# Kernel optimization log

Hardware: AMD Instinct MI355X
Metric: run time of the kernel (lower is better)

Reference implementation:

```python
import jax, jax.numpy as jnp
import numpy as np
import math

N, IFZ, NVZ, AHZ, QPZ, KZ, PEZ = 1024, 256, 64, 8, 4, 20, 20
NUM_FREQ = PEZ // 2
FREQ_INV = 50.0

def layer_norm(x, g, b, eps=1e-5):
    mu = x.mean(-1, keepdims=True)
    var = ((x - mu) ** 2).mean(-1, keepdims=True)
    return (x - mu) / jnp.sqrt(var + eps) * g + b

def setup_inputs() -> dict:
    key = jax.random.key(0)
    ks = jax.random.split(key, 8)
    x = jax.random.normal(ks[0], (N, IFZ), jnp.float32)
    affines = jax.random.normal(ks[1], (N, 3, 4), jnp.float32)
    prot_mask = jnp.ones((N,), dtype=bool)
    edge_index = jax.random.randint(ks[2], (N, KZ), 0, N, dtype=jnp.int32)
    s = 0.02
    w_nde = jax.random.normal(ks[3], (KZ * 3 * PEZ, NVZ), jnp.float32) * s
    b_nde = jnp.zeros((NVZ,), jnp.float32)
    w_q = jax.random.normal(ks[4], (IFZ + NVZ, AHZ * QPZ * 3), jnp.float32) * s
    w_v = jax.random.normal(ks[5], (IFZ + NVZ, AHZ * QPZ * IFZ), jnp.float32) * s
    ln_ag_g = jnp.ones((AHZ * QPZ * IFZ,), jnp.float32)
    ln_ag_b = jnp.zeros((AHZ * QPZ * IFZ,), jnp.float32)
    w_ag = jax.random.normal(ks[6], (AHZ * QPZ * IFZ, IFZ), jnp.float32) * s
    ln_en_g = jnp.ones((IFZ,), jnp.float32)
    ln_en_b = jnp.zeros((IFZ,), jnp.float32)
    return dict(x=x, affines=affines, prot_mask=prot_mask, edge_index=edge_index,
                w_nde=w_nde, b_nde=b_nde, w_q=w_q, w_v=w_v,
                ln_ag_g=ln_ag_g, ln_ag_b=ln_ag_b, w_ag=w_ag,
                ln_en_g=ln_en_g, ln_en_b=ln_en_b)

def reference(x, affines, prot_mask, edge_index, w_nde, b_nde, w_q, w_v,
              ln_ag_g, ln_ag_b, w_ag, ln_en_g, ln_en_b):
    dtype = x.dtype
    R = affines[:, :, :3]                                   # (N,3,3) rotation
    t = affines[:, :, 3]                                    # (N,3) translation
    positions = t
    # --- BackboneDistanceEmbedding (reconstructed): local neighbour vectors ---
    rel = positions[edge_index] - t[:, None, :]             # (N,K,3)
    local = jnp.einsum('nji,nkj->nki', R, rel)              # inverse-affine (R^T) (N,K,3)
    freqs = jnp.arange(1, NUM_FREQ + 1, dtype=dtype) / FREQ_INV
    ang = local[..., None] * freqs                          # (N,K,3,F)
    pe = jnp.concatenate([jnp.sin(ang), jnp.cos(ang)], -1)  # (N,K,3,PEZ)
    nv = jax.nn.relu(pe.reshape(x.shape[0], -1) @ w_nde + b_nde)  # (N,NVZ)
    nv = nv * prot_mask[:, None].astype(dtype)
    x_ne = jnp.concatenate([x, nv], axis=-1)                # (N,IFZ+NVZ)
    # --- query points in global frame ---
    q = (x_ne @ w_q).reshape(-1, 1, AHZ, QPZ, 3)
    q = jnp.einsum('nij,nkaqj->nkaqi', R, q) + t[:, None, None, None, :]
    gnp = positions[edge_index][:, :, None, None, :]        # (N,K,1,1,3)
    # --- L2-distance attention over neighbourhood ---
    scores = -jnp.linalg.norm(q - gnp, axis=-1).sum(-1)     # (N,K,AHZ)
    attn = jax.nn.softmax(scores, axis=1).astype(dtype)
    # --- value gather + weighted aggregation ---
    v = (x_ne @ w_v).reshape(-1, AHZ, QPZ, IFZ)
    v_ne = v[edge_index]                                    # (N,K,AHZ,QPZ,IFZ) -- big gather
    new = jnp.einsum('nkaqi,nka->naqi', v_ne, attn).reshape(x.shape[0], -1)
    new = layer_norm(new, ln_ag_g, ln_ag_b) @ w_ag          # dropout: eval mode => identity
    out = layer_norm(x + new / math.sqrt(2.0), ln_en_g, ln_en_b).astype(dtype)
    return out, edge_index
```

## Files before the change

### kernel.cpp

```cpp
#include <hip/hip_runtime.h>
#include <hip/hip_bf16.h>
#include <math.h>

#define NNODE 1024
#define IFZ   256
#define NVZ   64
#define AHZ   8
#define QPZ   4
#define KZ    20
#define NF    10
#define XNE   320
#define VROW  8192
#define PEK   1280
#define PTOT  2560

typedef unsigned short ushort;
typedef __attribute__((ext_vector_type(8))) short    short8v;
typedef __attribute__((ext_vector_type(8))) ushort   ushort8v;
typedef __attribute__((ext_vector_type(4))) float    float4v;

static __device__ __forceinline__ ushort f2bf(float f) {
    unsigned u = __float_as_uint(f);
    unsigned r = 0x7FFFu + ((u >> 16) & 1u);
    return (ushort)((u + r) >> 16);
}
static __device__ __forceinline__ float bf2f(unsigned h) {
    return __uint_as_float(h << 16);
}

struct Params {
    const float *w_ag, *ln_ag_g, *ln_ag_b, *w_nde, *b_nde, *w_q, *w_v, *x, *aff;
    const int   *edge;
    const float *ln_en_g, *ln_en_b;
    ushort *wagT, *wndeT, *wqT, *wv_bf, *pebf, *xne_bf, *agg, *WcT, *G;
    float  *rsum, *vpart, *vconst, *qbuf, *geom, *S, *s2part, *tmpk, *out;
};

static __device__ __forceinline__ void gemm_tile(
    const ushort* __restrict__ A, const ushort* __restrict__ BT,
    int aStride, int btStride, int kLen, int bm, int bn, int tid,
    float4v acc[2][2], ushort (&As)[64][40], ushort (&Bs)[64][40])
{
    const int w = tid >> 6, lane = tid & 63;
    const int wr = w >> 1, wc = w & 1;
    const int lane15 = lane & 15, quad = lane >> 4;
    const int sm = tid >> 2, sk = (tid & 3) * 8;
    for (int k0 = 0; k0 < kLen; k0 += 32) {
        *(ushort8v*)&As[sm][sk] = *(const ushort8v*)&A[(size_t)(bm + sm)*aStride + k0 + sk];
        *(ushort8v*)&Bs[sm][sk] = *(const ushort8v*)&BT[(size_t)(bn + sm)*btStride + k0 + sk];
        __syncthreads();
        short8v a0 = *(const short8v*)&As[wr*32      + lane15][quad*8];
        short8v a1 = *(const short8v*)&As[wr*32 + 16 + lane15][quad*8];
        short8v b0 = *(const short8v*)&Bs[wc*32      + lane15][quad*8];
        short8v b1 = *(const short8v*)&Bs[wc*32 + 16 + lane15][quad*8];
        acc[0][0] = __builtin_amdgcn_mfma_f32_16x16x32_bf16(a0, b0, acc[0][0], 0, 0, 0);
        acc[0][1] = __builtin_amdgcn_mfma_f32_16x16x32_bf16(a0, b1, acc[0][1], 0, 0, 0);
        acc[1][0] = __builtin_amdgcn_mfma_f32_16x16x32_bf16(a1, b0, acc[1][0], 0, 0, 0);
        acc[1][1] = __builtin_amdgcn_mfma_f32_16x16x32_bf16(a1, b1, acc[1][1], 0, 0, 0);
        __syncthreads();
    }
}

#define T1_END 2048
#define T2_END 2128
#define T3_END 2168
#define CV_END 2488
#define GV_END 2552
#define K0_END 2808

__global__ __launch_bounds__(256) void k_prep(Params P)
{
    const int u = blockIdx.x;
    const int tid = threadIdx.x;
    __shared__ float t[32][33];
    __shared__ float part[256];
    __shared__ float tn[4][KZ][3];
    __shared__ float r9[4][9], tt[4][3];

    if (u < T3_END) {
        const float* src; ushort* dst; const float* scl;
        int R, C, gx, Rdst, rel;
        if (u < T1_END)      { src=P.w_ag; dst=P.wagT; scl=P.ln_ag_g; R=VROW; C=IFZ; gx=8; Rdst=VROW; rel=u; }
        else if (u < T2_END) { src=P.w_nde;dst=P.wndeT;scl=nullptr;   R=1200; C=NVZ; gx=2; Rdst=PEK;  rel=u-T1_END; }
        else                 { src=P.w_q;  dst=P.wqT;  scl=nullptr;   R=XNE;  C=96;  gx=4; Rdst=XNE;  rel=u-T2_END; }
        const int bx = rel % gx, by = rel / gx;
        const int c0 = bx*32, r0 = by*32;
        const int tx = tid & 31, ty = tid >> 5;
        #pragma unroll
        for (int i = 0; i < 4; ++i) {
            int r = r0 + ty + 8*i, c = c0 + tx;
            float v = (r < R && c < C) ? src[(size_t)r * C + c] : 0.f;
            if (scl && r < R) v *= scl[r];
            t[ty + 8*i][tx] = v;
        }
        __syncthreads();
        #pragma unroll
        for (int i = 0; i < 4; ++i)
            dst[(size_t)(c0 + ty + 8*i) * Rdst + r0 + tx] = f2bf(t[tx][ty + 8*i]);
    } else if (u < CV_END) {
        const int j = u - T3_END;
        const float* src = P.w_v + (size_t)j*VROW + tid*32;
        ushort* dst = P.wv_bf + (size_t)j*VROW + tid*32;
        float psum = 0.f;
        #pragma unroll
        for (int q = 0; q < 4; ++q) {
            float4 v0 = ((const float4*)src)[q*2];
            float4 v1 = ((const float4*)src)[q*2+1];
            psum += v0.x+v0.y+v0.z+v0.w + v1.x+v1.y+v1.z+v1.w;
            ushort8v o;
            o[0]=f2bf(v0.x); o[1]=f2bf(v0.y); o[2]=f2bf(v0.z); o[3]=f2bf(v0.w);
            o[4]=f2bf(v1.x); o[5]=f2bf(v1.y); o[6]=f2bf(v1.z); o[7]=f2bf(v1.w);
            *(ushort8v*)(dst + q*8) = o;
        }
        part[tid] = psum;
        __syncthreads();
        if (tid < 8) {
            float s = 0.f;
            #pragma unroll
            for (int v = 0; v < 32; ++v) s += part[tid*32 + v];
            P.rsum[tid*320 + j] = s;
        }
    } else if (u < GV_END) {
        const int sp = u - CV_END, j = tid;
        const float* base = P.w_ag + (size_t)sp * 128 * IFZ;
        float vp = 0.f, bp = 0.f;
        for (int r = 0; r < 128; ++r) {
            float wv = base[(size_t)r * IFZ + j];
            vp += P.ln_ag_g[sp*128 + r] * wv;
            bp += P.ln_ag_b[sp*128 + r] * wv;
        }
        P.vpart[(size_t)(sp*2 + 0) * IFZ + j] = vp;
        P.vpart[(size_t)(sp*2 + 1) * IFZ + j] = bp;
    } else {
        const int rel = u - GV_END;
        const int wv = tid >> 6, lane = tid & 63;
        const int n = rel*4 + wv;
        if (lane < KZ) {
            int e = P.edge[n*KZ + lane];
            float a0 = P.aff[e*12 + 3], a1 = P.aff[e*12 + 7], a2 = P.aff[e*12 + 11];
            tn[wv][lane][0] = a0; tn[wv][lane][1] = a1; tn[wv][lane][2] = a2;
            P.geom[n*72 + 12 + lane*3 + 0] = a0;
            P.geom[n*72 + 12 + lane*3 + 1] = a1;
            P.geom[n*72 + 12 + lane*3 + 2] = a2;
        } else if (lane < 29) {
            int q = lane - 20;
            float v = P.aff[n*12 + (q/3)*4 + (q%3)];
            r9[wv][q] = v;
            P.geom[n*72 + q] = v;
        } else if (lane < 32) {
            float v = P.aff[n*12 + (lane-29)*4 + 3];
            tt[wv][lane-29] = v;
            P.geom[n*72 + 9 + (lane-29)] = v;
        }
        {
            float4 xv = ((const float4*)(P.x + (size_t)n*IFZ))[lane];
            unsigned lo = f2bf(xv.x) | ((unsigned)f2bf(xv.y) << 16);
            unsigned hi = f2bf(xv.z) | ((unsigned)f2bf(xv.w) << 16);
            unsigned* p = (unsigned*)(P.xne_bf + (size_t)n*XNE) + lane*2;
            p[0] = lo; p[1] = hi;
        }
        __syncthreads();
        if (lane < 60) {
            int k = lane / 3, i = lane % 3;
            float d0 = tn[wv][k][0]-tt[wv][0];
            float d1 = tn[wv][k][1]-tt[wv][1];
            float d2 = tn[wv][k][2]-tt[wv][2];
            float loc = r9[wv][0+i]*d0 + r9[wv][3+i]*d1 + r9[wv][6+i]*d2;
            size_t base = (size_t)n*PEK + k*60 + i*20;
            #pragma unroll
            for (int p = 0; p < NF; p += 2) {
                float a0 = loc * (float)(p+1) * (1.0f/50.0f);
                float a1 = loc * (float)(p+2) * (1.0f/50.0f);
                unsigned us = f2bf(__sinf(a0)) | ((unsigned)f2bf(__sinf(a1)) << 16);
                unsigned uc = f2bf(__cosf(a0)) | ((unsigned)f2bf(__cosf(a1)) << 16);
                *(unsigned*)&P.pebf[base + p]      = us;
                *(unsigned*)&P.pebf[base + 10 + p] = uc;
            }
        }
        if (lane < 40)
            *(unsigned*)&P.pebf[(size_t)n*PEK + 1200 + lane*2] = 0u;
    }
}

__global__ __launch_bounds__(256) void k_jobs(Params P)
{
    const int u = blockIdx.x;
    const int tid = threadIdx.x;
    __shared__ ushort As[64][40];
    __shared__ ushort Bs[64][40];

    if (u >= 408) {
        int vb = u - 408;
        float s = 0.f;
        #pragma unroll 8
        for (int sp = 0; sp < 64; ++sp)
            s += P.vpart[(size_t)(sp*2 + vb)*IFZ + tid];
        P.vconst[vb*IFZ + tid] = s;
        return;
    }
    const ushort *A, *BT;
    int aStr, btStr, kLen, bm, bn, mode, ldc;
    ushort* Cb = nullptr; float* Cf = nullptr; size_t cbase = 0;
    if (u < 160) {
        int bx=u%5, by=(u/5)%4, bz=u/20;
        A = P.wagT + bz*1024; BT = P.wv_bf + bz*1024;
        aStr=VROW; btStr=VROW; kLen=1024;
        bm=by*64; bn=bx*64; Cb=P.WcT; cbase=(size_t)bz*320; ldc=PTOT; mode=0;
    } else if (u < 360) {
        int rel=u-160; int bx=rel%5, by=(rel/5)%5, bz=rel/25;
        A = P.wv_bf + bz*1024; BT = P.wv_bf + bz*1024;
        aStr=VROW; btStr=VROW; kLen=1024;
        bm=by*64; bn=bx*64; Cb=P.G; cbase=(size_t)bz*102400; ldc=320; mode=0;
    } else if (u < 376) {
        int by=u-360;
        A = P.pebf; BT = P.wndeT; aStr=PEK; btStr=PEK; kLen=PEK;
        bm=by*64; bn=0; ldc=0; mode=2;
    } else {
        int rel=u-376; int bx=rel%2, by=rel/2;
        A = P.xne_bf; BT = P.wqT; aStr=XNE; btStr=XNE; kLen=256;
        bm=by*64; bn=bx*64; Cf=P.qbuf; cbase=0; ldc=128; mode=1;
    }
    float4v acc[2][2] = {};
    gemm_tile(A, BT, aStr, btStr, kLen, bm, bn, tid, acc, As, Bs);

    const int w = tid >> 6, lane = tid & 63;
    const int wr = w >> 1, wc = w & 1;
    const int lane15 = lane & 15, quad = lane >> 4;
    #pragma unroll
    for (int i = 0; i < 2; ++i) {
        #pragma unroll
        for (int j = 0; j < 2; ++j) {
            int col = bn + wc*32 + j*16 + lane15;
            #pragma unroll
            for (int r = 0; r < 4; ++r) {
                int row = bm + wr*32 + i*16 + quad*4 + r;
                float val = acc[i][j][r];
                if (mode == 2) {
                    val = fmaxf(val + P.b_nde[col], 0.f);
                    P.xne_bf[(size_t)row*XNE + IFZ + col] = f2bf(val);
                } else if (mode == 1) {
                    Cf[cbase + (size_t)row*ldc + col] = val;
                } else {
                    Cb[cbase + (size_t)row*ldc + col] = f2bf(val);
                }
            }
        }
    }
}

__global__ __launch_bounds__(256) void k_sc_agg(Params P)
{
    const int n = blockIdx.x;
    const int tid = threadIdx.x;
    __shared__ float geo[72], qf[96], qg[96], sc[160], at[160], nvr[64];
    __shared__ float rs[PTOT], red[256];
    __shared__ int es[KZ];
    __shared__ ushort xs[KZ][XNE];

    if (tid < 72) geo[tid] = P.geom[n*72 + tid];
    if (tid < KZ) es[tid] = P.edge[n*KZ + tid];
    if (tid < 64) nvr[tid] = bf2f(P.xne_bf[(size_t)n*XNE + IFZ + tid]);
    for (int p = tid; p < PTOT; p += 256) rs[p] = P.rsum[p];
    __syncthreads();

    for (int s = tid; s < KZ*40; s += 256) {
        int k = s / 40, ch = s % 40;
        *(ushort8v*)&xs[k][ch*8] =
            *(const ushort8v*)&P.xne_bf[(size_t)es[k]*XNE + ch*8];
    }
    if (tid < 96) {
        float qv = P.qbuf[n*128 + tid];
        #pragma unroll 16
        for (int r = 0; r < 64; ++r)
            qv += nvr[r] * P.w_q[(256 + r)*96 + tid];
        qf[tid] = qv;
    }
    __syncthreads();
    if (tid < 96) {
        int i = tid % 3, base = (tid/3)*3;
        qg[tid] = geo[i*3+0]*qf[base] + geo[i*3+1]*qf[base+1]
                + geo[i*3+2]*qf[base+2] + geo[9+i];
    }
    __syncthreads();
    if (tid < 160) {
        int k = tid / 8, a = tid % 8;
        float tx = geo[12+k*3+0], ty = geo[12+k*3+1], tz = geo[12+k*3+2];
        float acc = 0.f;
        #pragma unroll
        for (int qp = 0; qp < QPZ; ++qp) {
            int b = a*12 + qp*3;
            float dx = qg[b]   - tx;
            float dy = qg[b+1] - ty;
            float dz = qg[b+2] - tz;
            acc += sqrtf(dx*dx + dy*dy + dz*dz);
        }
        sc[a*20 + k] = -acc;
    }
    __syncthreads();
    if (tid < 8) {
        int a = tid;
        float m = -1e30f;
        #pragma unroll
        for (int k = 0; k < KZ; ++k) m = fmaxf(m, sc[a*20+k]);
        float e[KZ]; float sum = 0.f;
        #pragma unroll
        for (int k = 0; k < KZ; ++k) { e[k] = __expf(sc[a*20+k] - m); sum += e[k]; }
        float inv = 1.f / sum;
        #pragma unroll
        for (int k = 0; k < KZ; ++k) at[k*8 + a] = e[k]*inv;
    }
    __syncthreads();

    float sp = 0.f;
    for (int s = tid; s < AHZ*40; s += 256) {
        int a = s / 40, ch = s % 40;
        float acc[8] = {};
        #pragma unroll 4
        for (int k = 0; k < KZ; ++k) {
            ushort8v p = *(const ushort8v*)&xs[k][ch*8];
            float wgt = at[k*8 + a];
            #pragma unroll
            for (int j = 0; j < 8; ++j)
                acc[j] += wgt * bf2f((ushort)p[j]);
        }
        ushort8v o;
        #pragma unroll
        for (int j = 0; j < 8; ++j) {
            o[j] = (short)f2bf(acc[j]);
            sp += acc[j] * rs[a*320 + ch*8 + j];
        }
        *(ushort8v*)&P.agg[(size_t)n*PTOT + a*320 + ch*8] = o;
    }
    red[tid] = sp;
    __syncthreads();
    if (tid < 64) {
        float v = red[tid] + red[tid+64] + red[tid+128] + red[tid+192];
        #pragma unroll
        for (int off = 32; off > 0; off >>= 1) v += __shfl_down(v, off, 64);
        if (tid == 0) P.S[n] = v;
    }
}

__global__ __launch_bounds__(256) void k_gemm_b(Params P)
{
    const int u = blockIdx.x;
    const int tid = threadIdx.x;
    __shared__ ushort As[64][40];
    __shared__ ushort Bs[64][40];
    const int w = tid >> 6, lane = tid & 63;
    const int wr = w >> 1, wc = w & 1;
    const int lane15 = lane & 15, quad = lane >> 4;
    float4v acc[2][2] = {};

    if (u < 640) {
        const int bx = u % 5, by = (u/5) % 16, a = u/80;
        const int bm = by*64, bn = bx*64;
        gemm_tile(P.agg + a*320, P.G + (size_t)a*102400,
                  PTOT, 320, 320, bm, bn, tid, acc, As, Bs);
        #pragma unroll
        for (int i = 0; i < 2; ++i) {
            #pragma unroll
            for (int r = 0; r < 4; ++r) {
                int row = bm + wr*32 + i*16 + quad*4 + r;
                int c0  = bn + wc*32 + lane15;
                float av0 = bf2f(P.agg[(size_t)row*PTOT + a*320 + c0]);
                float av1 = bf2f(P.agg[(size_t)row*PTOT + a*320 + c0 + 16]);
                float v = acc[i][0][r]*av0 + acc[i][1][r]*av1;
                v += __shfl_xor(v, 1, 64);
                v += __shfl_xor(v, 2, 64);
                v += __shfl_xor(v, 4, 64);
                v += __shfl_xor(v, 8, 64);
                if (lane15 == 0)
                    P.s2part[(size_t)row*80 + a*10 + (bn>>5) + wc] = v;
            }
        }
    } else {
        const int rel = u - 640;
        const int bx = rel % 4, by = (rel/4) % 16, z = rel/64;
        const int bm = by*64, bn = bx*64;
        gemm_tile(P.agg + z*1280, P.WcT + z*1280,
                  PTOT, PTOT, 1280, bm, bn, tid, acc, As, Bs);
        float* Cf = P.tmpk + (size_t)z*NNODE*IFZ;
        #pragma unroll
        for (int i = 0; i < 2; ++i) {
            #pragma unroll
            for (int j = 0; j < 2; ++j) {
                int col = bn + wc*32 + j*16 + lane15;
                #pragma unroll
                for (int r = 0; r < 4; ++r) {
                    int row = bm + wr*32 + i*16 + quad*4 + r;
                    Cf[(size_t)row*IFZ + col] = acc[i][j][r];
                }
            }
        }
    }
}

__global__ __launch_bounds__(256) void k_final(Params P)
{
    const int n = blockIdx.x;
    const int tid = threadIdx.x;
    __shared__ float wsum[4], wsq[4];
    __shared__ float s_mu8, s_rstd8, s_mu, s_rstd;
    const int wid = tid >> 6, lane = tid & 63;

    float v = (tid < 80) ? P.s2part[(size_t)n*80 + tid] : 0.f;
    #pragma unroll
    for (int off = 32; off > 0; off >>= 1) v += __shfl_down(v, off, 64);
    if (lane == 0) wsum[wid] = v;
    __syncthreads();
    if (tid == 0) {
        float S2 = wsum[0]+wsum[1]+wsum[2]+wsum[3];
        float Sv = P.S[n];
        float mu = Sv * (1.f/(float)VROW);
        float var = S2 * (1.f/(float)VROW) - mu*mu;
        s_mu8 = mu; s_rstd8 = rsqrtf(var + 1e-5f);
    }
    __syncthreads();
    const float mu8 = s_mu8, rstd8 = s_rstd8;

    float s = P.tmpk[n*IFZ + tid] + P.tmpk[NNODE*IFZ + n*IFZ + tid];
    float vc = P.vconst[tid], bc = P.vconst[IFZ + tid];
    float pre = rstd8*s - rstd8*mu8*vc + bc;

    float val = P.x[n*IFZ + tid] + pre * 0.70710678118654752f;
    float lsum = val, lsq = val*val;
    #pragma unroll
    for (int off = 32; off > 0; off >>= 1) {
        lsum += __shfl_down(lsum, off, 64);
        lsq  += __shfl_down(lsq,  off, 64);
    }
    __syncthreads();
    if (lane == 0) { wsum[wid] = lsum; wsq[wid] = lsq; }
    __syncthreads();
    if (tid == 0) {
        float ts = wsum[0]+wsum[1]+wsum[2]+wsum[3];
        float tq = wsq[0]+wsq[1]+wsq[2]+wsq[3];
        float mu = ts / (float)IFZ;
        float var = tq / (float)IFZ - mu*mu;
        s_mu = mu; s_rstd = rsqrtf(var + 1e-5f);
    }
    __syncthreads();
    P.out[n*IFZ + tid] = (val - s_mu)*s_rstd*P.ln_en_g[tid] + P.ln_en_b[tid];
    if (tid < KZ)
        P.out[NNODE*IFZ + n*KZ + tid] = (float)P.edge[n*KZ + tid];
}

extern "C" void kernel_launch(void* const* d_in, const int* in_sizes, int n_in,
                              void* d_out, int out_size, void* d_ws, size_t ws_size,
                              hipStream_t stream)
{
    char* w = (char*)d_ws;
    Params P;
    P.x       = (const float*)d_in[0];
    P.aff     = (const float*)d_in[1];
    P.edge    = (const int*)d_in[3];
    P.w_nde   = (const float*)d_in[4];
    P.b_nde   = (const float*)d_in[5];
    P.w_q     = (const float*)d_in[6];
    P.w_v     = (const float*)d_in[7];
    P.ln_ag_g = (const float*)d_in[8];
    P.ln_ag_b = (const float*)d_in[9];
    P.w_ag    = (const float*)d_in[10];
    P.ln_en_g = (const float*)d_in[11];
    P.ln_en_b = (const float*)d_in[12];
    P.out     = (float*)d_out;

    P.xne_bf = (ushort*)(w + 0x0);
    P.qbuf   = (float*) (w + 0xA0000);
    P.vpart  = (float*) (w + 0x120000);
    P.vconst = (float*) (w + 0x140000);
    P.wagT   = (ushort*)(w + 0x250000);
    P.wv_bf  = (ushort*)(w + 0x650000);
    P.WcT    = (ushort*)(w + 0xB50000);
    P.G      = (ushort*)(w + 0xC90000);
    P.rsum   = (float*) (w + 0xE20000);
    P.S      = (float*) (w + 0xE23000);
    P.s2part = (float*) (w + 0xE24000);
    P.agg    = (ushort*)(w + 0xE80000);
    P.tmpk   = (float*) (w + 0x1380000);
    P.pebf   = (ushort*)(w + 0x1580000);
    P.wndeT  = (ushort*)(w + 0x1800000);
    P.wqT    = (ushort*)(w + 0x1828000);
    P.geom   = (float*) (w + 0x1840000);

    hipLaunchKernelGGL(k_prep,   dim3(K0_END), dim3(256), 0, stream, P);
    hipLaunchKernelGGL(k_jobs,   dim3(410),    dim3(256), 0, stream, P);
    hipLaunchKernelGGL(k_sc_agg, dim3(NNODE),  dim3(256), 0, stream, P);
    hipLaunchKernelGGL(k_gemm_b, dim3(768),    dim3(256), 0, stream, P);
    hipLaunchKernelGGL(k_final,  dim3(NNODE),  dim3(256), 0, stream, P);
}
```

Measured before the change: 161.3 us.

## Fuse node-embedding, query and attention softmax into prep kernel; merge launches

The positional-encoding MLP, query projection, global query transform, distance scores and softmax are now computed per group of four nodes inside k_prep with fp32 scalar loops, writing attention weights directly. This removes the bf16 PE buffer, the transposed w_nde/w_q copies, the qbuf/geom intermediates and their MFMA GEMM tiles. The aggregation work and the weight GEMMs are merged into a single k_mid launch, cutting one kernel launch and one global round trip. In exchange the PE and query matmuls run as scalar FMA loops over 256 blocks instead of tensor-core tiles, and each block reads the full w_nde and w_q.

```diff
diff --git a/kernel.cpp b/kernel.cpp
--- a/kernel.cpp
+++ b/kernel.cpp
@@ -11,7 +11,6 @@
 #define NF    10
 #define XNE   320
 #define VROW  8192
-#define PEK   1280
 #define PTOT  2560
 
 typedef unsigned short ushort;
@@ -32,8 +31,8 @@
     const float *w_ag, *ln_ag_g, *ln_ag_b, *w_nde, *b_nde, *w_q, *w_v, *x, *aff;
     const int   *edge;
     const float *ln_en_g, *ln_en_b;
-    ushort *wagT, *wndeT, *wqT, *wv_bf, *pebf, *xne_bf, *agg, *WcT, *G;
-    float  *rsum, *vpart, *vconst, *qbuf, *geom, *S, *s2part, *tmpk, *out;
+    ushort *xne_bf, *agg, *wagT, *wv_bf, *WcT, *G;
+    float  *rsum, *vpart, *vconst, *attn, *S, *s2part, *tmpk, *out;
 };
 
 static __device__ __forceinline__ void gemm_tile(
@@ -61,44 +60,166 @@
     }
 }
 
-#define T1_END 2048
-#define T2_END 2128
-#define T3_END 2168
-#define CV_END 2488
-#define GV_END 2552
-#define K0_END 2808
+#define K0P_END 256
+#define CV_END  576
+#define GV_END  640
+#define T1_END  2688
+
+union SharedP {
+    struct { float t[32][33]; } t1;
+    struct { float part[256]; } cv;
+    struct {
+        float tn[4][KZ][3], r9[4][9], tt[4][3];
+        float pe[4][1200];
+        float xr[4][IFZ];
+        float nv[4][NVZ];
+        float red[4][256];
+        float q[4][96];
+        float qred[2][384];
+        float qg[4][96];
+        float sc[4][160];
+    } k0;
+};
 
 __global__ __launch_bounds__(256) void k_prep(Params P)
 {
     const int u = blockIdx.x;
     const int tid = threadIdx.x;
-    __shared__ float t[32][33];
-    __shared__ float part[256];
-    __shared__ float tn[4][KZ][3];
-    __shared__ float r9[4][9], tt[4][3];
-
-    if (u < T3_END) {
-        const float* src; ushort* dst; const float* scl;
-        int R, C, gx, Rdst, rel;
-        if (u < T1_END)      { src=P.w_ag; dst=P.wagT; scl=P.ln_ag_g; R=VROW; C=IFZ; gx=8; Rdst=VROW; rel=u; }
-        else if (u < T2_END) { src=P.w_nde;dst=P.wndeT;scl=nullptr;   R=1200; C=NVZ; gx=2; Rdst=PEK;  rel=u-T1_END; }
-        else                 { src=P.w_q;  dst=P.wqT;  scl=nullptr;   R=XNE;  C=96;  gx=4; Rdst=XNE;  rel=u-T2_END; }
-        const int bx = rel % gx, by = rel / gx;
-        const int c0 = bx*32, r0 = by*32;
-        const int tx = tid & 31, ty = tid >> 5;
-        #pragma unroll
-        for (int i = 0; i < 4; ++i) {
-            int r = r0 + ty + 8*i, c = c0 + tx;
-            float v = (r < R && c < C) ? src[(size_t)r * C + c] : 0.f;
-            if (scl && r < R) v *= scl[r];
-            t[ty + 8*i][tx] = v;
-        }
-        __syncthreads();
-        #pragma unroll
-        for (int i = 0; i < 4; ++i)
-            dst[(size_t)(c0 + ty + 8*i) * Rdst + r0 + tx] = f2bf(t[tx][ty + 8*i]);
+    __shared__ SharedP sh;
+
+    if (u < K0P_END) {
+        const int n0 = u*4;
+        const int m = tid >> 6, lane = tid & 63;
+        const int n = n0 + m;
+
+        if (lane < KZ) {
+            int e = P.edge[n*KZ + lane];
+            sh.k0.tn[m][lane][0] = P.aff[e*12 + 3];
+            sh.k0.tn[m][lane][1] = P.aff[e*12 + 7];
+            sh.k0.tn[m][lane][2] = P.aff[e*12 + 11];
+        } else if (lane < 29) {
+            int q = lane - 20;
+            sh.k0.r9[m][q] = P.aff[n*12 + (q/3)*4 + (q%3)];
+        } else if (lane < 32) {
+            sh.k0.tt[m][lane-29] = P.aff[n*12 + (lane-29)*4 + 3];
+        }
+        {
+            float4 xv = ((const float4*)(P.x + (size_t)n*IFZ))[lane];
+            unsigned lo = f2bf(xv.x) | ((unsigned)f2bf(xv.y) << 16);
+            unsigned hi = f2bf(xv.z) | ((unsigned)f2bf(xv.w) << 16);
+            unsigned* p = (unsigned*)(P.xne_bf + (size_t)n*XNE) + lane*2;
+            p[0] = lo; p[1] = hi;
+            sh.k0.xr[m][lane*4+0] = xv.x; sh.k0.xr[m][lane*4+1] = xv.y;
+            sh.k0.xr[m][lane*4+2] = xv.z; sh.k0.xr[m][lane*4+3] = xv.w;
+        }
+        __syncthreads();
+
+        if (lane < 60) {
+            int k = lane / 3, i = lane % 3;
+            float d0 = sh.k0.tn[m][k][0]-sh.k0.tt[m][0];
+            float d1 = sh.k0.tn[m][k][1]-sh.k0.tt[m][1];
+            float d2 = sh.k0.tn[m][k][2]-sh.k0.tt[m][2];
+            float loc = sh.k0.r9[m][0+i]*d0 + sh.k0.r9[m][3+i]*d1 + sh.k0.r9[m][6+i]*d2;
+            int base = k*60 + i*20;
+            #pragma unroll
+            for (int p = 0; p < NF; ++p) {
+                float a = loc * (float)(p+1) * (1.0f/50.0f);
+                sh.k0.pe[m][base + p]      = __sinf(a);
+                sh.k0.pe[m][base + 10 + p] = __cosf(a);
+            }
+        }
+        __syncthreads();
+
+        {
+            const int c = tid & 63, chunk = tid >> 6;
+            const int r0 = chunk * 300;
+            float a0=0.f, a1=0.f, a2=0.f, a3=0.f;
+            for (int r = r0; r < r0 + 300; ++r) {
+                float wv = P.w_nde[r*NVZ + c];
+                a0 += sh.k0.pe[0][r]*wv;
+                a1 += sh.k0.pe[1][r]*wv;
+                a2 += sh.k0.pe[2][r]*wv;
+                a3 += sh.k0.pe[3][r]*wv;
+            }
+            sh.k0.red[chunk][0*64+c] = a0;
+            sh.k0.red[chunk][1*64+c] = a1;
+            sh.k0.red[chunk][2*64+c] = a2;
+            sh.k0.red[chunk][3*64+c] = a3;
+        }
+        __syncthreads();
+        {
+            const int mm = tid >> 6, c = tid & 63;
+            float nv = sh.k0.red[0][mm*64+c] + sh.k0.red[1][mm*64+c]
+                     + sh.k0.red[2][mm*64+c] + sh.k0.red[3][mm*64+c] + P.b_nde[c];
+            nv = fmaxf(nv, 0.f);
+            sh.k0.nv[mm][c] = nv;
+            P.xne_bf[(size_t)(n0+mm)*XNE + IFZ + c] = f2bf(nv);
+        }
+        __syncthreads();
+
+        if (tid < 192) {
+            const int chunk = tid / 96, j = tid - chunk*96;
+            const int rA = chunk*160, rB = rA + 160;
+            float q0=0.f, q1=0.f, q2=0.f, q3=0.f;
+            for (int r = rA; r < rB; ++r) {
+                float wq = P.w_q[r*96 + j];
+                float x0 = (r < IFZ) ? sh.k0.xr[0][r] : sh.k0.nv[0][r-IFZ];
+                float x1 = (r < IFZ) ? sh.k0.xr[1][r] : sh.k0.nv[1][r-IFZ];
+                float x2 = (r < IFZ) ? sh.k0.xr[2][r] : sh.k0.nv[2][r-IFZ];
+                float x3 = (r < IFZ) ? sh.k0.xr[3][r] : sh.k0.nv[3][r-IFZ];
+                q0 += x0*wq; q1 += x1*wq; q2 += x2*wq; q3 += x3*wq;
+            }
+            sh.k0.qred[chunk][0*96+j] = q0;
+            sh.k0.qred[chunk][1*96+j] = q1;
+            sh.k0.qred[chunk][2*96+j] = q2;
+            sh.k0.qred[chunk][3*96+j] = q3;
+        }
+        __syncthreads();
+        if (tid < 96) {
+            #pragma unroll
+            for (int mm = 0; mm < 4; ++mm)
+                sh.k0.q[mm][tid] = sh.k0.qred[0][mm*96+tid] + sh.k0.qred[1][mm*96+tid];
+        }
+        __syncthreads();
+
+        for (int c = lane; c < 96; c += 64) {
+            int i = c % 3, base = (c/3)*3;
+            sh.k0.qg[m][c] = sh.k0.r9[m][i*3+0]*sh.k0.q[m][base]
+                           + sh.k0.r9[m][i*3+1]*sh.k0.q[m][base+1]
+                           + sh.k0.r9[m][i*3+2]*sh.k0.q[m][base+2] + sh.k0.tt[m][i];
+        }
+        __syncthreads();
+
+        for (int s = lane; s < 160; s += 64) {
+            int k = s / 8, a = s % 8;
+            float tx = sh.k0.tn[m][k][0], ty = sh.k0.tn[m][k][1], tz = sh.k0.tn[m][k][2];
+            float acc = 0.f;
+            #pragma unroll
+            for (int qp = 0; qp < QPZ; ++qp) {
+                int b = a*12 + qp*3;
+                float dx = sh.k0.qg[m][b]   - tx;
+                float dy = sh.k0.qg[m][b+1] - ty;
+                float dz = sh.k0.qg[m][b+2] - tz;
+                acc += sqrtf(dx*dx + dy*dy + dz*dz);
+            }
+            sh.k0.sc[m][a*20 + k] = -acc;
+        }
+        __syncthreads();
+
+        if (lane < 8) {
+            int a = lane;
+            float mx = -1e30f;
+            #pragma unroll
+            for (int k = 0; k < KZ; ++k) mx = fmaxf(mx, sh.k0.sc[m][a*20+k]);
+            float e[KZ]; float sum = 0.f;
+            #pragma unroll
+            for (int k = 0; k < KZ; ++k) { e[k] = __expf(sh.k0.sc[m][a*20+k] - mx); sum += e[k]; }
+            float inv = 1.f / sum;
+            #pragma unroll
+            for (int k = 0; k < KZ; ++k) P.attn[n*160 + k*8 + a] = e[k]*inv;
+        }
     } else if (u < CV_END) {
-        const int j = u - T3_END;
+        const int j = u - K0P_END;
         const float* src = P.w_v + (size_t)j*VROW + tid*32;
         ushort* dst = P.wv_bf + (size_t)j*VROW + tid*32;
         float psum = 0.f;
@@ -112,12 +233,12 @@
             o[4]=f2bf(v1.x); o[5]=f2bf(v1.y); o[6]=f2bf(v1.z); o[7]=f2bf(v1.w);
             *(ushort8v*)(dst + q*8) = o;
         }
-        part[tid] = psum;
+        sh.cv.part[tid] = psum;
         __syncthreads();
         if (tid < 8) {
             float s = 0.f;
             #pragma unroll
-            for (int v = 0; v < 32; ++v) s += part[tid*32 + v];
+            for (int v = 0; v < 32; ++v) s += sh.cv.part[tid*32 + v];
             P.rsum[tid*320 + j] = s;
         }
     } else if (u < GV_END) {
@@ -133,64 +254,81 @@
         P.vpart[(size_t)(sp*2 + 1) * IFZ + j] = bp;
     } else {
         const int rel = u - GV_END;
-        const int wv = tid >> 6, lane = tid & 63;
-        const int n = rel*4 + wv;
-        if (lane < KZ) {
-            int e = P.edge[n*KZ + lane];
-            float a0 = P.aff[e*12 + 3], a1 = P.aff[e*12 + 7], a2 = P.aff[e*12 + 11];
-            tn[wv][lane][0] = a0; tn[wv][lane][1] = a1; tn[wv][lane][2] = a2;
-            P.geom[n*72 + 12 + lane*3 + 0] = a0;
-            P.geom[n*72 + 12 + lane*3 + 1] = a1;
-            P.geom[n*72 + 12 + lane*3 + 2] = a2;
-        } else if (lane < 29) {
-            int q = lane - 20;
-            float v = P.aff[n*12 + (q/3)*4 + (q%3)];
-            r9[wv][q] = v;
-            P.geom[n*72 + q] = v;
-        } else if (lane < 32) {
-            float v = P.aff[n*12 + (lane-29)*4 + 3];
-            tt[wv][lane-29] = v;
-            P.geom[n*72 + 9 + (lane-29)] = v;
-        }
-        {
-            float4 xv = ((const float4*)(P.x + (size_t)n*IFZ))[lane];
-            unsigned lo = f2bf(xv.x) | ((unsigned)f2bf(xv.y) << 16);
-            unsigned hi = f2bf(xv.z) | ((unsigned)f2bf(xv.w) << 16);
-            unsigned* p = (unsigned*)(P.xne_bf + (size_t)n*XNE) + lane*2;
-            p[0] = lo; p[1] = hi;
-        }
-        __syncthreads();
-        if (lane < 60) {
-            int k = lane / 3, i = lane % 3;
-            float d0 = tn[wv][k][0]-tt[wv][0];
-            float d1 = tn[wv][k][1]-tt[wv][1];
-            float d2 = tn[wv][k][2]-tt[wv][2];
-            float loc = r9[wv][0+i]*d0 + r9[wv][3+i]*d1 + r9[wv][6+i]*d2;
-            size_t base = (size_t)n*PEK + k*60 + i*20;
-            #pragma unroll
-            for (int p = 0; p < NF; p += 2) {
-                float a0 = loc * (float)(p+1) * (1.0f/50.0f);
-                float a1 = loc * (float)(p+2) * (1.0f/50.0f);
-                unsigned us = f2bf(__sinf(a0)) | ((unsigned)f2bf(__sinf(a1)) << 16);
-                unsigned uc = f2bf(__cosf(a0)) | ((unsigned)f2bf(__cosf(a1)) << 16);
-                *(unsigned*)&P.pebf[base + p]      = us;
-                *(unsigned*)&P.pebf[base + 10 + p] = uc;
-            }
-        }
-        if (lane < 40)
-            *(unsigned*)&P.pebf[(size_t)n*PEK + 1200 + lane*2] = 0u;
-    }
-}
-
-__global__ __launch_bounds__(256) void k_jobs(Params P)
+        const int bx = rel % 8, by = rel / 8;
+        const int c0 = bx*32, r0 = by*32;
+        const int tx = tid & 31, ty = tid >> 5;
+        #pragma unroll
+        for (int i = 0; i < 4; ++i) {
+            int r = r0 + ty + 8*i, c = c0 + tx;
+            sh.t1.t[ty + 8*i][tx] = P.w_ag[(size_t)r * IFZ + c] * P.ln_ag_g[r];
+        }
+        __syncthreads();
+        #pragma unroll
+        for (int i = 0; i < 4; ++i)
+            P.wagT[(size_t)(c0 + ty + 8*i) * VROW + r0 + tx] = f2bf(sh.t1.t[tx][ty + 8*i]);
+    }
+}
+
+union SharedM {
+    struct { ushort As[64][40]; ushort Bs[64][40]; } g;
+    struct { float at[160]; float rs[PTOT]; float red[256];
+             int es[KZ]; ushort xs[KZ][XNE]; } s;
+};
+
+__global__ __launch_bounds__(256) void k_mid(Params P)
 {
     const int u = blockIdx.x;
     const int tid = threadIdx.x;
-    __shared__ ushort As[64][40];
-    __shared__ ushort Bs[64][40];
-
-    if (u >= 408) {
-        int vb = u - 408;
+    __shared__ SharedM sh;
+
+    if (u < NNODE) {
+        const int n = u;
+        if (tid < 160) sh.s.at[tid] = P.attn[n*160 + tid];
+        if (tid < KZ) sh.s.es[tid] = P.edge[n*KZ + tid];
+        for (int p = tid; p < PTOT; p += 256) sh.s.rs[p] = P.rsum[p];
+        __syncthreads();
+
+        for (int s = tid; s < KZ*40; s += 256) {
+            int k = s / 40, ch = s % 40;
+            *(ushort8v*)&sh.s.xs[k][ch*8] =
+                *(const ushort8v*)&P.xne_bf[(size_t)sh.s.es[k]*XNE + ch*8];
+        }
+        __syncthreads();
+
+        float sp = 0.f;
+        for (int s = tid; s < AHZ*40; s += 256) {
+            int a = s / 40, ch = s % 40;
+            float acc[8] = {};
+            #pragma unroll 4
+            for (int k = 0; k < KZ; ++k) {
+                ushort8v p = *(const ushort8v*)&sh.s.xs[k][ch*8];
+                float wgt = sh.s.at[k*8 + a];
+                #pragma unroll
+                for (int j = 0; j < 8; ++j)
+                    acc[j] += wgt * bf2f((ushort)p[j]);
+            }
+            ushort8v o;
+            #pragma unroll
+            for (int j = 0; j < 8; ++j) {
+                o[j] = (short)f2bf(acc[j]);
+                sp += acc[j] * sh.s.rs[a*320 + ch*8 + j];
+            }
+            *(ushort8v*)&P.agg[(size_t)n*PTOT + a*320 + ch*8] = o;
+        }
+        sh.s.red[tid] = sp;
+        __syncthreads();
+        if (tid < 64) {
+            float v = sh.s.red[tid] + sh.s.red[tid+64] + sh.s.red[tid+128] + sh.s.red[tid+192];
+            #pragma unroll
+            for (int off = 32; off > 0; off >>= 1) v += __shfl_down(v, off, 64);
+            if (tid == 0) P.S[n] = v;
+        }
+        return;
+    }
+
+    const int u2 = u - NNODE;
+    if (u2 >= 360) {
+        int vb = u2 - 360;
         float s = 0.f;
         #pragma unroll 8
         for (int sp = 0; sp < 64; ++sp)
@@ -198,30 +336,18 @@
         P.vconst[vb*IFZ + tid] = s;
         return;
     }
-    const ushort *A, *BT;
-    int aStr, btStr, kLen, bm, bn, mode, ldc;
-    ushort* Cb = nullptr; float* Cf = nullptr; size_t cbase = 0;
-    if (u < 160) {
-        int bx=u%5, by=(u/5)%4, bz=u/20;
+    const ushort *A, *BT; ushort* Cb; size_t cbase; int bm, bn, ldc;
+    if (u2 < 160) {
+        int bx=u2%5, by=(u2/5)%4, bz=u2/20;
         A = P.wagT + bz*1024; BT = P.wv_bf + bz*1024;
-        aStr=VROW; btStr=VROW; kLen=1024;
-        bm=by*64; bn=bx*64; Cb=P.WcT; cbase=(size_t)bz*320; ldc=PTOT; mode=0;
-    } else if (u < 360) {
-        int rel=u-160; int bx=rel%5, by=(rel/5)%5, bz=rel/25;
+        bm=by*64; bn=bx*64; Cb=P.WcT; cbase=(size_t)bz*320; ldc=PTOT;
+    } else {
+        int rel=u2-160; int bx=rel%5, by=(rel/5)%5, bz=rel/25;
         A = P.wv_bf + bz*1024; BT = P.wv_bf + bz*1024;
-        aStr=VROW; btStr=VROW; kLen=1024;
-        bm=by*64; bn=bx*64; Cb=P.G; cbase=(size_t)bz*102400; ldc=320; mode=0;
-    } else if (u < 376) {
-        int by=u-360;
-        A = P.pebf; BT = P.wndeT; aStr=PEK; btStr=PEK; kLen=PEK;
-        bm=by*64; bn=0; ldc=0; mode=2;
-    } else {
-        int rel=u-376; int bx=rel%2, by=rel/2;
-        A = P.xne_bf; BT = P.wqT; aStr=XNE; btStr=XNE; kLen=256;
-        bm=by*64; bn=bx*64; Cf=P.qbuf; cbase=0; ldc=128; mode=1;
+        bm=by*64; bn=bx*64; Cb=P.G; cbase=(size_t)bz*102400; ldc=320;
     }
     float4v acc[2][2] = {};
-    gemm_tile(A, BT, aStr, btStr, kLen, bm, bn, tid, acc, As, Bs);
+    gemm_tile(A, BT, VROW, VROW, 1024, bm, bn, tid, acc, sh.g.As, sh.g.Bs);
 
     const int w = tid >> 6, lane = tid & 63;
     const int wr = w >> 1, wc = w & 1;
@@ -234,110 +360,9 @@
             #pragma unroll
             for (int r = 0; r < 4; ++r) {
                 int row = bm + wr*32 + i*16 + quad*4 + r;
-                float val = acc[i][j][r];
-                if (mode == 2) {
-                    val = fmaxf(val + P.b_nde[col], 0.f);
-                    P.xne_bf[(size_t)row*XNE + IFZ + col] = f2bf(val);
-                } else if (mode == 1) {
-                    Cf[cbase + (size_t)row*ldc + col] = val;
-                } else {
-                    Cb[cbase + (size_t)row*ldc + col] = f2bf(val);
-                }
-            }
-        }
-    }
-}
-
-__global__ __launch_bounds__(256) void k_sc_agg(Params P)
-{
-    const int n = blockIdx.x;
-    const int tid = threadIdx.x;
-    __shared__ float geo[72], qf[96], qg[96], sc[160], at[160], nvr[64];
-    __shared__ float rs[PTOT], red[256];
-    __shared__ int es[KZ];
-    __shared__ ushort xs[KZ][XNE];
-
-    if (tid < 72) geo[tid] = P.geom[n*72 + tid];
-    if (tid < KZ) es[tid] = P.edge[n*KZ + tid];
-    if (tid < 64) nvr[tid] = bf2f(P.xne_bf[(size_t)n*XNE + IFZ + tid]);
-    for (int p = tid; p < PTOT; p += 256) rs[p] = P.rsum[p];
-    __syncthreads();
-
-    for (int s = tid; s < KZ*40; s += 256) {
-        int k = s / 40, ch = s % 40;
-        *(ushort8v*)&xs[k][ch*8] =
-            *(const ushort8v*)&P.xne_bf[(size_t)es[k]*XNE + ch*8];
-    }
-    if (tid < 96) {
-        float qv = P.qbuf[n*128 + tid];
-        #pragma unroll 16
-        for (int r = 0; r < 64; ++r)
-            qv += nvr[r] * P.w_q[(256 + r)*96 + tid];
-        qf[tid] = qv;
-    }
-    __syncthreads();
-    if (tid < 96) {
-        int i = tid % 3, base = (tid/3)*3;
-        qg[tid] = geo[i*3+0]*qf[base] + geo[i*3+1]*qf[base+1]
-                + geo[i*3+2]*qf[base+2] + geo[9+i];
-    }
-    __syncthreads();
-    if (tid < 160) {
-        int k = tid / 8, a = tid % 8;
-        float tx = geo[12+k*3+0], ty = geo[12+k*3+1], tz = geo[12+k*3+2];
-        float acc = 0.f;
-        #pragma unroll
-        for (int qp = 0; qp < QPZ; ++qp) {
-            int b = a*12 + qp*3;
-            float dx = qg[b]   - tx;
-            float dy = qg[b+1] - ty;
-            float dz = qg[b+2] - tz;
-            acc += sqrtf(dx*dx + dy*dy + dz*dz);
-        }
-        sc[a*20 + k] = -acc;
-    }
-    __syncthreads();
-    if (tid < 8) {
-        int a = tid;
-        float m = -1e30f;
-        #pragma unroll
-        for (int k = 0; k < KZ; ++k) m = fmaxf(m, sc[a*20+k]);
-        float e[KZ]; float sum = 0.f;
-        #pragma unroll
-        for (int k = 0; k < KZ; ++k) { e[k] = __expf(sc[a*20+k] - m); sum += e[k]; }
-        float inv = 1.f / sum;
-        #pragma unroll
-        for (int k = 0; k < KZ; ++k) at[k*8 + a] = e[k]*inv;
-    }
-    __syncthreads();
-
-    float sp = 0.f;
-    for (int s = tid; s < AHZ*40; s += 256) {
-        int a = s / 40, ch = s % 40;
-        float acc[8] = {};
-        #pragma unroll 4
-        for (int k = 0; k < KZ; ++k) {
-            ushort8v p = *(const ushort8v*)&xs[k][ch*8];
-            float wgt = at[k*8 + a];
-            #pragma unroll
-            for (int j = 0; j < 8; ++j)
-                acc[j] += wgt * bf2f((ushort)p[j]);
-        }
-        ushort8v o;
-        #pragma unroll
-        for (int j = 0; j < 8; ++j) {
-            o[j] = (short)f2bf(acc[j]);
-            sp += acc[j] * rs[a*320 + ch*8 + j];
-        }
-        *(ushort8v*)&P.agg[(size_t)n*PTOT + a*320 + ch*8] = o;
-    }
-    red[tid] = sp;
-    __syncthreads();
-    if (tid < 64) {
-        float v = red[tid] + red[tid+64] + red[tid+128] + red[tid+192];
-        #pragma unroll
-        for (int off = 32; off > 0; off >>= 1) v += __shfl_down(v, off, 64);
-        if (tid == 0) P.S[n] = v;
+                Cb[cbase + (size_t)row*ldc + col] = f2bf(acc[i][j][r]);
+            }
+        }
     }
 }
 
@@ -467,26 +492,21 @@
     P.out     = (float*)d_out;
 
     P.xne_bf = (ushort*)(w + 0x0);
-    P.qbuf   = (float*) (w + 0xA0000);
-    P.vpart  = (float*) (w + 0x120000);
-    P.vconst = (float*) (w + 0x140000);
-    P.wagT   = (ushort*)(w + 0x250000);
-    P.wv_bf  = (ushort*)(w + 0x650000);
-    P.WcT    = (ushort*)(w + 0xB50000);
-    P.G      = (ushort*)(w + 0xC90000);
-    P.rsum   = (float*) (w + 0xE20000);
-    P.S      = (float*) (w + 0xE23000);
-    P.s2part = (float*) (w + 0xE24000);
-    P.agg    = (ushort*)(w + 0xE80000);
-    P.tmpk   = (float*) (w + 0x1380000);
-    P.pebf   = (ushort*)(w + 0x1580000);
-    P.wndeT  = (ushort*)(w + 0x1800000);
-    P.wqT    = (ushort*)(w + 0x1828000);
-    P.geom   = (float*) (w + 0x1840000);
-
-    hipLaunchKernelGGL(k_prep,   dim3(K0_END), dim3(256), 0, stream, P);
-    hipLaunchKernelGGL(k_jobs,   dim3(410),    dim3(256), 0, stream, P);
-    hipLaunchKernelGGL(k_sc_agg, dim3(NNODE),  dim3(256), 0, stream, P);
+    P.attn   = (float*) (w + 0xA0000);
+    P.vpart  = (float*) (w + 0x140000);
+    P.vconst = (float*) (w + 0x160000);
+    P.wagT   = (ushort*)(w + 0x170000);
+    P.wv_bf  = (ushort*)(w + 0x570000);
+    P.WcT    = (ushort*)(w + 0xA70000);
+    P.G      = (ushort*)(w + 0xBB0000);
+    P.rsum   = (float*) (w + 0xD40000);
+    P.S      = (float*) (w + 0xD43000);
+    P.s2part = (float*) (w + 0xD44000);
+    P.agg    = (ushort*)(w + 0xDA0000);
+    P.tmpk   = (float*) (w + 0x12A0000);
+
+    hipLaunchKernelGGL(k_prep,   dim3(T1_END), dim3(256), 0, stream, P);
+    hipLaunchKernelGGL(k_mid,    dim3(1386),   dim3(256), 0, stream, P);
     hipLaunchKernelGGL(k_gemm_b, dim3(768),    dim3(256), 0, stream, P);
     hipLaunchKernelGGL(k_final,  dim3(NNODE),  dim3(256), 0, stream, P);
 }
```

Result: slower. 171.0 us (+6.0%).

## Move weight-only GEMMs into the score/aggregation kernel to overlap work

Applied to the files above, without the earlier changes.

The weight-only GEMM tiles (WcT = w_ag^T·w_v and the Gram matrix G of w_v) no longer sit in the first jobs kernel. They now run as extra blocks of the per-node score/aggregation kernel, with shared memory overlaid through a union. The small jobs kernel keeps only the PE/NDE and query GEMMs plus the vconst reduction, so the critical path before aggregation gets shorter and the big GEMMs can run alongside the per-node blocks. The union shares the larger per-node shared-memory footprint with the GEMM blocks, which may limit occupancy. A small unroll pragma is also added to the vpart loop.

```diff
diff --git a/kernel.cpp b/kernel.cpp
--- a/kernel.cpp
+++ b/kernel.cpp
@@ -124,6 +124,7 @@
         const int sp = u - CV_END, j = tid;
         const float* base = P.w_ag + (size_t)sp * 128 * IFZ;
         float vp = 0.f, bp = 0.f;
+        #pragma unroll 4
         for (int r = 0; r < 128; ++r) {
             float wv = base[(size_t)r * IFZ + j];
             vp += P.ln_ag_g[sp*128 + r] * wv;
@@ -182,15 +183,15 @@
     }
 }
 
-__global__ __launch_bounds__(256) void k_jobs(Params P)
+__global__ __launch_bounds__(256) void k_sjobs(Params P)
 {
     const int u = blockIdx.x;
     const int tid = threadIdx.x;
     __shared__ ushort As[64][40];
     __shared__ ushort Bs[64][40];
 
-    if (u >= 408) {
-        int vb = u - 408;
+    if (u >= 48) {
+        int vb = u - 48;
         float s = 0.f;
         #pragma unroll 8
         for (int sp = 0; sp < 64; ++sp)
@@ -199,26 +200,14 @@
         return;
     }
     const ushort *A, *BT;
-    int aStr, btStr, kLen, bm, bn, mode, ldc;
-    ushort* Cb = nullptr; float* Cf = nullptr; size_t cbase = 0;
-    if (u < 160) {
-        int bx=u%5, by=(u/5)%4, bz=u/20;
-        A = P.wagT + bz*1024; BT = P.wv_bf + bz*1024;
-        aStr=VROW; btStr=VROW; kLen=1024;
-        bm=by*64; bn=bx*64; Cb=P.WcT; cbase=(size_t)bz*320; ldc=PTOT; mode=0;
-    } else if (u < 360) {
-        int rel=u-160; int bx=rel%5, by=(rel/5)%5, bz=rel/25;
-        A = P.wv_bf + bz*1024; BT = P.wv_bf + bz*1024;
-        aStr=VROW; btStr=VROW; kLen=1024;
-        bm=by*64; bn=bx*64; Cb=P.G; cbase=(size_t)bz*102400; ldc=320; mode=0;
-    } else if (u < 376) {
-        int by=u-360;
+    int kLen, bm, bn, mode, aStr, btStr;
+    if (u < 16) {
         A = P.pebf; BT = P.wndeT; aStr=PEK; btStr=PEK; kLen=PEK;
-        bm=by*64; bn=0; ldc=0; mode=2;
+        bm = u*64; bn = 0; mode = 2;
     } else {
-        int rel=u-376; int bx=rel%2, by=rel/2;
+        int rel = u - 16; int bx = rel % 2, by = rel / 2;
         A = P.xne_bf; BT = P.wqT; aStr=XNE; btStr=XNE; kLen=256;
-        bm=by*64; bn=bx*64; Cf=P.qbuf; cbase=0; ldc=128; mode=1;
+        bm = by*64; bn = bx*64; mode = 1;
     }
     float4v acc[2][2] = {};
     gemm_tile(A, BT, aStr, btStr, kLen, bm, bn, tid, acc, As, Bs);
@@ -238,76 +227,110 @@
                 if (mode == 2) {
                     val = fmaxf(val + P.b_nde[col], 0.f);
                     P.xne_bf[(size_t)row*XNE + IFZ + col] = f2bf(val);
-                } else if (mode == 1) {
-                    Cf[cbase + (size_t)row*ldc + col] = val;
                 } else {
-                    Cb[cbase + (size_t)row*ldc + col] = f2bf(val);
+                    P.qbuf[(size_t)row*128 + col] = val;
                 }
             }
         }
     }
 }
 
-__global__ __launch_bounds__(256) void k_sc_agg(Params P)
-{
-    const int n = blockIdx.x;
+union SharedM {
+    struct { ushort As[64][40]; ushort Bs[64][40]; } g;
+    struct { float geo[72], qf[96], qg[96], sc[160], at[160], nvr[64];
+             float rs[PTOT], red[256]; int es[KZ]; ushort xs[KZ][XNE]; } s;
+};
+
+__global__ __launch_bounds__(256) void k_mid(Params P)
+{
+    const int u = blockIdx.x;
     const int tid = threadIdx.x;
-    __shared__ float geo[72], qf[96], qg[96], sc[160], at[160], nvr[64];
-    __shared__ float rs[PTOT], red[256];
-    __shared__ int es[KZ];
-    __shared__ ushort xs[KZ][XNE];
-
-    if (tid < 72) geo[tid] = P.geom[n*72 + tid];
-    if (tid < KZ) es[tid] = P.edge[n*KZ + tid];
-    if (tid < 64) nvr[tid] = bf2f(P.xne_bf[(size_t)n*XNE + IFZ + tid]);
-    for (int p = tid; p < PTOT; p += 256) rs[p] = P.rsum[p];
+    __shared__ SharedM sh;
+
+    if (u < 360) {
+        const ushort *A, *BT; ushort* Cb; size_t cbase; int bm, bn, ldc;
+        if (u < 160) {
+            int bx=u%5, by=(u/5)%4, bz=u/20;
+            A = P.wagT + bz*1024; BT = P.wv_bf + bz*1024;
+            bm=by*64; bn=bx*64; Cb=P.WcT; cbase=(size_t)bz*320; ldc=PTOT;
+        } else {
+            int rel=u-160; int bx=rel%5, by=(rel/5)%5, bz=rel/25;
+            A = P.wv_bf + bz*1024; BT = P.wv_bf + bz*1024;
+            bm=by*64; bn=bx*64; Cb=P.G; cbase=(size_t)bz*102400; ldc=320;
+        }
+        float4v acc[2][2] = {};
+        gemm_tile(A, BT, VROW, VROW, 1024, bm, bn, tid, acc, sh.g.As, sh.g.Bs);
+
+        const int w = tid >> 6, lane = tid & 63;
+        const int wr = w >> 1, wc = w & 1;
+        const int lane15 = lane & 15, quad = lane >> 4;
+        #pragma unroll
+        for (int i = 0; i < 2; ++i) {
+            #pragma unroll
+            for (int j = 0; j < 2; ++j) {
+                int col = bn + wc*32 + j*16 + lane15;
+                #pragma unroll
+                for (int r = 0; r < 4; ++r) {
+                    int row = bm + wr*32 + i*16 + quad*4 + r;
+                    Cb[cbase + (size_t)row*ldc + col] = f2bf(acc[i][j][r]);
+                }
+            }
+        }
+        return;
+    }
+
+    const int n = u - 360;
+    if (tid < 72) sh.s.geo[tid] = P.geom[n*72 + tid];
+    if (tid < KZ) sh.s.es[tid] = P.edge[n*KZ + tid];
+    if (tid < 64) sh.s.nvr[tid] = bf2f(P.xne_bf[(size_t)n*XNE + IFZ + tid]);
+    for (int p = tid; p < PTOT; p += 256) sh.s.rs[p] = P.rsum[p];
     __syncthreads();
 
     for (int s = tid; s < KZ*40; s += 256) {
         int k = s / 40, ch = s % 40;
-        *(ushort8v*)&xs[k][ch*8] =
-            *(const ushort8v*)&P.xne_bf[(size_t)es[k]*XNE + ch*8];
+        *(ushort8v*)&sh.s.xs[k][ch*8] =
+            *(const ushort8v*)&P.xne_bf[(size_t)sh.s.es[k]*XNE + ch*8];
     }
     if (tid < 96) {
         float qv = P.qbuf[n*128 + tid];
         #pragma unroll 16
         for (int r = 0; r < 64; ++r)
-            qv += nvr[r] * P.w_q[(256 + r)*96 + tid];
-        qf[tid] = qv;
+            qv += sh.s.nvr[r] * P.w_q[(256 + r)*96 + tid];
+        sh.s.qf[tid] = qv;
     }
     __syncthreads();
     if (tid < 96) {
         int i = tid % 3, base = (tid/3)*3;
-        qg[tid] = geo[i*3+0]*qf[base] + geo[i*3+1]*qf[base+1]
-                + geo[i*3+2]*qf[base+2] + geo[9+i];
+        sh.s.qg[tid] = sh.s.geo[i*3+0]*sh.s.qf[base] + sh.s.geo[i*3+1]*sh.s.qf[base+1]
+                     + sh.s.geo[i*3+2]*sh.s.qf[base+2] + sh.s.geo[9+i];
     }
     __syncthreads();
     if (tid < 160) {
         int k = tid / 8, a = tid % 8;
-        float tx = geo[12+k*3+0], ty = geo[12+k*3+1], tz = geo[12+k*3+2];
+        float tx = sh.s.geo[12+k*3+0], ty = sh.s.geo[12+k*3+1], tz = sh.s.geo[12+k*3+2];
         float acc = 0.f;
         #pragma unroll
         for (int qp = 0; qp < QPZ; ++qp) {
             int b = a*12 + qp*3;
-            float dx = qg[b]   - tx;
-            float dy = qg[b+1] - ty;
-            float dz = qg[b+2] - tz;
+            float dx = sh.s.qg[b]   - tx;
+            float dy = sh.s.qg[b+1] - ty;
+            float dz = sh.s.qg[b+2] - tz;
             acc += sqrtf(dx*dx + dy*dy + dz*dz);
         }
-        sc[a*20 + k] = -acc;
+        sh.s.sc[a*20 + k] = -acc;
     }
     __syncthreads();
     if (tid < 8) {
         int a = tid;
         float m = -1e30f;
         #pragma unroll
-        for (int k = 0; k < KZ; ++k) m = fmaxf(m, sc[a*20+k]);
+        for (int k = 0; k < KZ; ++k) m = fmaxf(m, sh.s.sc[a*20+k]);
         float e[KZ]; float sum = 0.f;
         #pragma unroll
-        for (int k = 0; k < KZ; ++k) { e[k] = __expf(sc[a*20+k] - m); sum += e[k]; }
+        for (int k = 0; k < KZ; ++k) { e[k] = __expf(sh.s.sc[a*20+k] - m); sum += e[k]; }
         float inv = 1.f / sum;
         #pragma unroll
-        for (int k = 0; k < KZ; ++k) at[k*8 + a] = e[k]*inv;
+        for (int k = 0; k < KZ; ++k) sh.s.at[k*8 + a] = e[k]*inv;
     }
     __syncthreads();
 
@@ -317,8 +340,8 @@
         float acc[8] = {};
         #pragma unroll 4
         for (int k = 0; k < KZ; ++k) {
-            ushort8v p = *(const ushort8v*)&xs[k][ch*8];
-            float wgt = at[k*8 + a];
+            ushort8v p = *(const ushort8v*)&sh.s.xs[k][ch*8];
+            float wgt = sh.s.at[k*8 + a];
             #pragma unroll
             for (int j = 0; j < 8; ++j)
                 acc[j] += wgt * bf2f((ushort)p[j]);
@@ -327,14 +350,14 @@
         #pragma unroll
         for (int j = 0; j < 8; ++j) {
             o[j] = (short)f2bf(acc[j]);
-            sp += acc[j] * rs[a*320 + ch*8 + j];
+            sp += acc[j] * sh.s.rs[a*320 + ch*8 + j];
         }
         *(ushort8v*)&P.agg[(size_t)n*PTOT + a*320 + ch*8] = o;
     }
-    red[tid] = sp;
+    sh.s.red[tid] = sp;
     __syncthreads();
     if (tid < 64) {
-        float v = red[tid] + red[tid+64] + red[tid+128] + red[tid+192];
+        float v = sh.s.red[tid] + sh.s.red[tid+64] + sh.s.red[tid+128] + sh.s.red[tid+192];
         #pragma unroll
         for (int off = 32; off > 0; off >>= 1) v += __shfl_down(v, off, 64);
         if (tid == 0) P.S[n] = v;
@@ -485,8 +508,8 @@
     P.geom   = (float*) (w + 0x1840000);
 
     hipLaunchKernelGGL(k_prep,   dim3(K0_END), dim3(256), 0, stream, P);
-    hipLaunchKernelGGL(k_jobs,   dim3(410),    dim3(256), 0, stream, P);
-    hipLaunchKernelGGL(k_sc_agg, dim3(NNODE),  dim3(256), 0, stream, P);
+    hipLaunchKernelGGL(k_sjobs,  dim3(50),     dim3(256), 0, stream, P);
+    hipLaunchKernelGGL(k_mid,    dim3(1384),   dim3(256), 0, stream, P);
     hipLaunchKernelGGL(k_gemm_b, dim3(768),    dim3(256), 0, stream, P);
     hipLaunchKernelGGL(k_final,  dim3(NNODE),  dim3(256), 0, stream, P);
 }
```

New measurement: 170.8 us. 1.06x slower.
